# Kernel optimization log

Measured on AMD Instinct MI355X. Metric: run time of the kernel, lower is better.

The kernel has to match this reference:

```python
import jax, jax.numpy as jnp
import numpy as np

B, T = 8192, 2048


def setup_inputs() -> dict:
    key = jax.random.key(0)
    u = jax.random.normal(key, (B, T, 1), dtype=jnp.float32)
    return {
        "u": u,
        "dt": jnp.float32(0.01),
        "m": jnp.float32(1.0),
        "c": jnp.float32(0.1),
        "k": jnp.float32(2.0),
        "in_mean": jnp.float32(0.5),
        "in_std": jnp.float32(2.0),
        "out_mean": jnp.float32(0.0),
        "out_std": jnp.float32(1.5),
    }


def reference(u, dt, m, c, k, in_mean, in_std, out_mean, out_std):
    # u: (B, T, 1) scaled forcing signal; state: (B, 2) = [position, velocity]
    Bsz = u.shape[0]
    u_seq = jnp.transpose(u[..., 0])  # (T, B) for lax.scan over time
    state0 = jnp.zeros((Bsz, 2), dtype=u.dtype)

    def step(state, u_t):
        # in_s.inverse_transform: unscale input
        u_p = u_t * in_std + in_mean  # (B,)
        x, v = state[:, 0], state[:, 1]
        # prior(state, u_p): mass-spring-damper derivative [dx, dv]
        acc = (u_p - c * v - k * x) / m
        new_state = state + dt * jnp.stack([v, acc], axis=1)  # Euler step
        # prior.ay on the UPDATED state (matches torch: state updated first)
        ay = (u_p - c * new_state[:, 1] - k * new_state[:, 0]) / m
        # out_s.transform: scale output
        y = (ay - out_mean) / out_std  # (B,)
        return new_state, y

    state_T, ys = jax.lax.scan(step, state0, u_seq)  # ys: (T, B)
    return jnp.transpose(ys), state_T  # (B, T), (B, 2)
```

## Files before the change

kernel.cpp:

```cpp
#include <hip/hip_runtime.h>

#define TT 2048
#define LP 32

__device__ __forceinline__ float b2f(unsigned short h) {
    union { unsigned int u; float f; } x; x.u = ((unsigned int)h) << 16; return x.f;
}
__device__ __forceinline__ unsigned short f2b(float f) {
    union { float f; unsigned int u; } x; x.f = f;
    unsigned int r = x.u + 0x7fffu + ((x.u >> 16) & 1u);
    return (unsigned short)(r >> 16);
}
__device__ __forceinline__ float ldsc(const void* p, bool bf) {
    return bf ? b2f(*(const unsigned short*)p) : *(const float*)p;
}
__device__ __forceinline__ int swz(int u) { return u ^ ((u >> 3) & 7); }

__global__ __launch_bounds__(256, 4) void phys_scan(
    const void* __restrict__ u_in,
    const void* __restrict__ p_dt, const void* __restrict__ p_m,
    const void* __restrict__ p_c,  const void* __restrict__ p_k,
    const void* __restrict__ p_im, const void* __restrict__ p_is,
    const void* __restrict__ p_om, const void* __restrict__ p_os,
    void* __restrict__ out, int rows)
{
    __shared__ uint4 smem[4][512];
    const int lane = threadIdx.x & 63;
    const int wid  = threadIdx.x >> 6;
    const int b = blockIdx.x * 4 + wid;
    if (b >= rows) return;

    uint4* W = smem[wid];

    const bool bf = (((const unsigned short*)p_m)[0] != 0);

    if (bf) {
        const uint4* g = (const uint4*)((const unsigned short*)u_in + (size_t)b * TT);
        #pragma unroll
        for (int j = 0; j < 4; j++) {
            uint4 w = g[j * 64 + lane];
            W[swz(j * 64 + lane)] = w;
        }
    } else {
        const uint4* g = (const uint4*)((const float*)u_in + (size_t)b * TT);
        #pragma unroll
        for (int j = 0; j < 8; j++) {
            uint4 w = g[j * 64 + lane];
            W[swz(j * 64 + lane)] = w;
        }
    }

    const float dt = ldsc(p_dt, bf);
    const float mm = ldsc(p_m,  bf);
    const float cc = ldsc(p_c,  bf);
    const float kk = ldsc(p_k,  bf);
    const float im = ldsc(p_im, bf);
    const float is = ldsc(p_is, bf);
    const float om = ldsc(p_om, bf);
    const float os = ldsc(p_os, bf);

    const float inv_m  = 1.0f / mm;
    const float inv_os = 1.0f / os;
    const float a21 = -dt * kk * inv_m;
    const float a22 = 1.0f - dt * cc * inv_m;
    const float dtm = dt * inv_m;

    __builtin_amdgcn_wave_barrier();
    float uf[LP];
    if (bf) {
        #pragma unroll
        for (int m = 0; m < 4; m++) {
            uint4 w = W[swz(lane * 4 + m)];
            unsigned int ws[4] = {w.x, w.y, w.z, w.w};
            #pragma unroll
            for (int q = 0; q < 4; q++) {
                uf[m*8 + q*2 + 0] = b2f((unsigned short)(ws[q] & 0xffffu));
                uf[m*8 + q*2 + 1] = b2f((unsigned short)(ws[q] >> 16));
            }
        }
    } else {
        #pragma unroll
        for (int m = 0; m < 8; m++) {
            uint4 w = W[swz(lane * 8 + m)];
            uf[m*4+0] = __uint_as_float(w.x);
            uf[m*4+1] = __uint_as_float(w.y);
            uf[m*4+2] = __uint_as_float(w.z);
            uf[m*4+3] = __uint_as_float(w.w);
        }
    }

    float px = 0.f, pv = 0.f;
    #pragma unroll
    for (int i = 0; i < LP; i++) {
        float up = uf[i] * is + im;
        uf[i] = up;
        float nx = px + dt * pv;
        float nv = a21 * px + a22 * pv + dtm * up;
        px = nx; pv = nv;
    }

    float m00 = 1.f, m01 = dt, m10 = a21, m11 = a22;
    #pragma unroll
    for (int i = 0; i < 5; i++) {
        float t00 = m00*m00 + m01*m10;
        float t01 = m00*m01 + m01*m11;
        float t10 = m10*m00 + m11*m10;
        float t11 = m10*m01 + m11*m11;
        m00=t00; m01=t01; m10=t10; m11=t11;
    }

    #pragma unroll
    for (int o = 1; o < 64; o <<= 1) {
        float rx = __shfl_up(px, o, 64);
        float rv = __shfl_up(pv, o, 64);
        if (lane >= o) {
            px = m00*rx + m01*rv + px;
            pv = m10*rx + m11*rv + pv;
        }
        if (o < 32) {
            float t00 = m00*m00 + m01*m10;
            float t01 = m00*m01 + m01*m11;
            float t10 = m10*m00 + m11*m10;
            float t11 = m10*m01 + m11*m11;
            m00=t00; m01=t01; m10=t10; m11=t11;
        }
    }

    float ex = __shfl_up(px, 1, 64);
    float ev = __shfl_up(pv, 1, 64);
    if (lane == 0) { ex = 0.f; ev = 0.f; }

    float x = ex, v = ev;
    #pragma unroll
    for (int i = 0; i < LP; i++) {
        float up = uf[i];
        float nx = x + dt * v;
        float nv = a21 * x + a22 * v + dtm * up;
        float ay = (up - cc * nv - kk * nx) * inv_m;
        uf[i] = (ay - om) * inv_os;
        x = nx; v = nv;
    }

    __builtin_amdgcn_wave_barrier();
    if (bf) {
        #pragma unroll
        for (int m = 0; m < 4; m++) {
            uint4 w;
            w.x = (unsigned)f2b(uf[m*8+0]) | ((unsigned)f2b(uf[m*8+1]) << 16);
            w.y = (unsigned)f2b(uf[m*8+2]) | ((unsigned)f2b(uf[m*8+3]) << 16);
            w.z = (unsigned)f2b(uf[m*8+4]) | ((unsigned)f2b(uf[m*8+5]) << 16);
            w.w = (unsigned)f2b(uf[m*8+6]) | ((unsigned)f2b(uf[m*8+7]) << 16);
            W[swz(lane * 4 + m)] = w;
        }
        __builtin_amdgcn_wave_barrier();
        unsigned short* ob = (unsigned short*)out;
        uint4* g = (uint4*)(ob + (size_t)b * TT);
        #pragma unroll
        for (int j = 0; j < 4; j++) g[j * 64 + lane] = W[swz(j * 64 + lane)];
        if (lane == 63) {
            size_t so = (size_t)rows * TT + (size_t)b * 2;
            ob[so]   = f2b(px);
            ob[so+1] = f2b(pv);
        }
    } else {
        #pragma unroll
        for (int m = 0; m < 8; m++) {
            uint4 w;
            w.x = __float_as_uint(uf[m*4+0]);
            w.y = __float_as_uint(uf[m*4+1]);
            w.z = __float_as_uint(uf[m*4+2]);
            w.w = __float_as_uint(uf[m*4+3]);
            W[swz(lane * 8 + m)] = w;
        }
        __builtin_amdgcn_wave_barrier();
        float* of = (float*)out;
        uint4* g = (uint4*)(of + (size_t)b * TT);
        #pragma unroll
        for (int j = 0; j < 8; j++) g[j * 64 + lane] = W[swz(j * 64 + lane)];
        if (lane == 63) {
            size_t so = (size_t)rows * TT + (size_t)b * 2;
            of[so]   = px;
            of[so+1] = pv;
        }
    }
}

extern "C" void kernel_launch(void* const* d_in, const int* in_sizes, int n_in,
                              void* d_out, int out_size, void* d_ws, size_t ws_size,
                              hipStream_t stream) {
    const int rows = in_sizes[0] / TT;
    const int blocks = (rows + 3) / 4;
    hipLaunchKernelGGL(phys_scan, dim3(blocks), dim3(256), 0, stream,
                       d_in[0], d_in[1], d_in[2], d_in[3], d_in[4],
                       d_in[5], d_in[6], d_in[7], d_in[8],
                       d_out, rows);
}
```

Before: 134.3 us.

## Make waves persistent over two rows with register prefetch of next row

After: 177.2 us. +32.0%, slower.

```diff
diff --git a/kernel.cpp b/kernel.cpp
--- a/kernel.cpp
+++ b/kernel.cpp
@@ -1,7 +1,6 @@
 #include <hip/hip_runtime.h>
 
 #define TT 2048
-#define LP 32
 
 __device__ __forceinline__ float b2f(unsigned short h) {
     union { unsigned int u; float f; } x; x.u = ((unsigned int)h) << 16; return x.f;
@@ -15,6 +14,163 @@
     return bf ? b2f(*(const unsigned short*)p) : *(const float*)p;
 }
 __device__ __forceinline__ int swz(int u) { return u ^ ((u >> 3) & 7); }
+
+template<bool BF>
+__device__ __forceinline__ void run_all(
+    const void* __restrict__ u_in, void* __restrict__ out, int rows,
+    int row0, int stride, int lane, uint4* __restrict__ W,
+    float dt, float cc, float kk, float inv_m,
+    float im, float is, float om, float inv_os)
+{
+    constexpr int NLD = BF ? 4 : 8;
+    constexpr int ES  = BF ? 2 : 4;
+
+    const float a21 = -dt * kk * inv_m;
+    const float a22 = 1.0f - dt * cc * inv_m;
+    const float dtm = dt * inv_m;
+
+    const char* ubase = (const char*)u_in;
+    char*       obase = (char*)out;
+
+    uint4 pf[NLD];
+    {
+        const uint4* g = (const uint4*)(ubase + (size_t)row0 * TT * ES);
+        #pragma unroll
+        for (int j = 0; j < NLD; j++) pf[j] = g[j * 64 + lane];
+    }
+
+    for (int r = row0; r < rows; r += stride) {
+        const int rn = r + stride;
+
+        __builtin_amdgcn_wave_barrier();
+        #pragma unroll
+        for (int j = 0; j < NLD; j++) W[swz(j * 64 + lane)] = pf[j];
+        __builtin_amdgcn_wave_barrier();
+
+        if (rn < rows) {
+            const uint4* g = (const uint4*)(ubase + (size_t)rn * TT * ES);
+            #pragma unroll
+            for (int j = 0; j < NLD; j++) pf[j] = g[j * 64 + lane];
+        }
+
+        float uf[32];
+        if (BF) {
+            #pragma unroll
+            for (int m = 0; m < 4; m++) {
+                uint4 w = W[swz(lane * 4 + m)];
+                unsigned int ws[4] = {w.x, w.y, w.z, w.w};
+                #pragma unroll
+                for (int q = 0; q < 4; q++) {
+                    uf[m*8 + q*2 + 0] = b2f((unsigned short)(ws[q] & 0xffffu));
+                    uf[m*8 + q*2 + 1] = b2f((unsigned short)(ws[q] >> 16));
+                }
+            }
+        } else {
+            #pragma unroll
+            for (int m = 0; m < 8; m++) {
+                uint4 w = W[swz(lane * 8 + m)];
+                uf[m*4+0] = __uint_as_float(w.x);
+                uf[m*4+1] = __uint_as_float(w.y);
+                uf[m*4+2] = __uint_as_float(w.z);
+                uf[m*4+3] = __uint_as_float(w.w);
+            }
+        }
+
+        float px = 0.f, pv = 0.f;
+        #pragma unroll
+        for (int i = 0; i < 32; i++) {
+            float up = uf[i] * is + im;
+            uf[i] = up;
+            float nx = px + dt * pv;
+            float nv = a21 * px + a22 * pv + dtm * up;
+            px = nx; pv = nv;
+        }
+
+        float m00 = 1.f, m01 = dt, m10 = a21, m11 = a22;
+        #pragma unroll
+        for (int i = 0; i < 5; i++) {
+            float t00 = m00*m00 + m01*m10;
+            float t01 = m00*m01 + m01*m11;
+            float t10 = m10*m00 + m11*m10;
+            float t11 = m10*m01 + m11*m11;
+            m00=t00; m01=t01; m10=t10; m11=t11;
+        }
+
+        #pragma unroll
+        for (int o = 1; o < 64; o <<= 1) {
+            float rx = __shfl_up(px, o, 64);
+            float rv = __shfl_up(pv, o, 64);
+            if (lane >= o) {
+                px = m00*rx + m01*rv + px;
+                pv = m10*rx + m11*rv + pv;
+            }
+            if (o < 32) {
+                float t00 = m00*m00 + m01*m10;
+                float t01 = m00*m01 + m01*m11;
+                float t10 = m10*m00 + m11*m10;
+                float t11 = m10*m01 + m11*m11;
+                m00=t00; m01=t01; m10=t10; m11=t11;
+            }
+        }
+
+        float ex = __shfl_up(px, 1, 64);
+        float ev = __shfl_up(pv, 1, 64);
+        if (lane == 0) { ex = 0.f; ev = 0.f; }
+
+        float x = ex, v = ev;
+        #pragma unroll
+        for (int i = 0; i < 32; i++) {
+            float up = uf[i];
+            float nx = x + dt * v;
+            float nv = a21 * x + a22 * v + dtm * up;
+            float ay = (up - cc * nv - kk * nx) * inv_m;
+            uf[i] = (ay - om) * inv_os;
+            x = nx; v = nv;
+        }
+
+        __builtin_amdgcn_wave_barrier();
+        if (BF) {
+            #pragma unroll
+            for (int m = 0; m < 4; m++) {
+                uint4 w;
+                w.x = (unsigned)f2b(uf[m*8+0]) | ((unsigned)f2b(uf[m*8+1]) << 16);
+                w.y = (unsigned)f2b(uf[m*8+2]) | ((unsigned)f2b(uf[m*8+3]) << 16);
+                w.z = (unsigned)f2b(uf[m*8+4]) | ((unsigned)f2b(uf[m*8+5]) << 16);
+                w.w = (unsigned)f2b(uf[m*8+6]) | ((unsigned)f2b(uf[m*8+7]) << 16);
+                W[swz(lane * 4 + m)] = w;
+            }
+        } else {
+            #pragma unroll
+            for (int m = 0; m < 8; m++) {
+                uint4 w;
+                w.x = __float_as_uint(uf[m*4+0]);
+                w.y = __float_as_uint(uf[m*4+1]);
+                w.z = __float_as_uint(uf[m*4+2]);
+                w.w = __float_as_uint(uf[m*4+3]);
+                W[swz(lane * 8 + m)] = w;
+            }
+        }
+        __builtin_amdgcn_wave_barrier();
+        {
+            uint4* g = (uint4*)(obase + (size_t)r * TT * ES);
+            #pragma unroll
+            for (int j = 0; j < NLD; j++) g[j * 64 + lane] = W[swz(j * 64 + lane)];
+        }
+        if (lane == 63) {
+            if (BF) {
+                unsigned short* ob = (unsigned short*)out;
+                size_t so = (size_t)rows * TT + (size_t)r * 2;
+                ob[so]   = f2b(px);
+                ob[so+1] = f2b(pv);
+            } else {
+                float* of = (float*)out;
+                size_t so = (size_t)rows * TT + (size_t)r * 2;
+                of[so]   = px;
+                of[so+1] = pv;
+            }
+        }
+    }
+}
 
 __global__ __launch_bounds__(256, 4) void phys_scan(
     const void* __restrict__ u_in,
@@ -22,33 +178,15 @@
     const void* __restrict__ p_c,  const void* __restrict__ p_k,
     const void* __restrict__ p_im, const void* __restrict__ p_is,
     const void* __restrict__ p_om, const void* __restrict__ p_os,
-    void* __restrict__ out, int rows)
+    void* __restrict__ out, int rows, int stride)
 {
     __shared__ uint4 smem[4][512];
     const int lane = threadIdx.x & 63;
     const int wid  = threadIdx.x >> 6;
-    const int b = blockIdx.x * 4 + wid;
-    if (b >= rows) return;
-
-    uint4* W = smem[wid];
+    const int row0 = blockIdx.x * 4 + wid;
+    if (row0 >= rows) return;
 
     const bool bf = (((const unsigned short*)p_m)[0] != 0);
-
-    if (bf) {
-        const uint4* g = (const uint4*)((const unsigned short*)u_in + (size_t)b * TT);
-        #pragma unroll
-        for (int j = 0; j < 4; j++) {
-            uint4 w = g[j * 64 + lane];
-            W[swz(j * 64 + lane)] = w;
-        }
-    } else {
-        const uint4* g = (const uint4*)((const float*)u_in + (size_t)b * TT);
-        #pragma unroll
-        for (int j = 0; j < 8; j++) {
-            uint4 w = g[j * 64 + lane];
-            W[swz(j * 64 + lane)] = w;
-        }
-    }
 
     const float dt = ldsc(p_dt, bf);
     const float mm = ldsc(p_m,  bf);
@@ -58,140 +196,25 @@
     const float is = ldsc(p_is, bf);
     const float om = ldsc(p_om, bf);
     const float os = ldsc(p_os, bf);
-
     const float inv_m  = 1.0f / mm;
     const float inv_os = 1.0f / os;
-    const float a21 = -dt * kk * inv_m;
-    const float a22 = 1.0f - dt * cc * inv_m;
-    const float dtm = dt * inv_m;
-
-    __builtin_amdgcn_wave_barrier();
-    float uf[LP];
-    if (bf) {
-        #pragma unroll
-        for (int m = 0; m < 4; m++) {
-            uint4 w = W[swz(lane * 4 + m)];
-            unsigned int ws[4] = {w.x, w.y, w.z, w.w};
-            #pragma unroll
-            for (int q = 0; q < 4; q++) {
-                uf[m*8 + q*2 + 0] = b2f((unsigned short)(ws[q] & 0xffffu));
-                uf[m*8 + q*2 + 1] = b2f((unsigned short)(ws[q] >> 16));
-            }
-        }
-    } else {
-        #pragma unroll
-        for (int m = 0; m < 8; m++) {
-            uint4 w = W[swz(lane * 8 + m)];
-            uf[m*4+0] = __uint_as_float(w.x);
-            uf[m*4+1] = __uint_as_float(w.y);
-            uf[m*4+2] = __uint_as_float(w.z);
-            uf[m*4+3] = __uint_as_float(w.w);
-        }
-    }
-
-    float px = 0.f, pv = 0.f;
-    #pragma unroll
-    for (int i = 0; i < LP; i++) {
-        float up = uf[i] * is + im;
-        uf[i] = up;
-        float nx = px + dt * pv;
-        float nv = a21 * px + a22 * pv + dtm * up;
-        px = nx; pv = nv;
-    }
-
-    float m00 = 1.f, m01 = dt, m10 = a21, m11 = a22;
-    #pragma unroll
-    for (int i = 0; i < 5; i++) {
-        float t00 = m00*m00 + m01*m10;
-        float t01 = m00*m01 + m01*m11;
-        float t10 = m10*m00 + m11*m10;
-        float t11 = m10*m01 + m11*m11;
-        m00=t00; m01=t01; m10=t10; m11=t11;
-    }
-
-    #pragma unroll
-    for (int o = 1; o < 64; o <<= 1) {
-        float rx = __shfl_up(px, o, 64);
-        float rv = __shfl_up(pv, o, 64);
-        if (lane >= o) {
-            px = m00*rx + m01*rv + px;
-            pv = m10*rx + m11*rv + pv;
-        }
-        if (o < 32) {
-            float t00 = m00*m00 + m01*m10;
-            float t01 = m00*m01 + m01*m11;
-            float t10 = m10*m00 + m11*m10;
-            float t11 = m10*m01 + m11*m11;
-            m00=t00; m01=t01; m10=t10; m11=t11;
-        }
-    }
-
-    float ex = __shfl_up(px, 1, 64);
-    float ev = __shfl_up(pv, 1, 64);
-    if (lane == 0) { ex = 0.f; ev = 0.f; }
-
-    float x = ex, v = ev;
-    #pragma unroll
-    for (int i = 0; i < LP; i++) {
-        float up = uf[i];
-        float nx = x + dt * v;
-        float nv = a21 * x + a22 * v + dtm * up;
-        float ay = (up - cc * nv - kk * nx) * inv_m;
-        uf[i] = (ay - om) * inv_os;
-        x = nx; v = nv;
-    }
-
-    __builtin_amdgcn_wave_barrier();
-    if (bf) {
-        #pragma unroll
-        for (int m = 0; m < 4; m++) {
-            uint4 w;
-            w.x = (unsigned)f2b(uf[m*8+0]) | ((unsigned)f2b(uf[m*8+1]) << 16);
-            w.y = (unsigned)f2b(uf[m*8+2]) | ((unsigned)f2b(uf[m*8+3]) << 16);
-            w.z = (unsigned)f2b(uf[m*8+4]) | ((unsigned)f2b(uf[m*8+5]) << 16);
-            w.w = (unsigned)f2b(uf[m*8+6]) | ((unsigned)f2b(uf[m*8+7]) << 16);
-            W[swz(lane * 4 + m)] = w;
-        }
-        __builtin_amdgcn_wave_barrier();
-        unsigned short* ob = (unsigned short*)out;
-        uint4* g = (uint4*)(ob + (size_t)b * TT);
-        #pragma unroll
-        for (int j = 0; j < 4; j++) g[j * 64 + lane] = W[swz(j * 64 + lane)];
-        if (lane == 63) {
-            size_t so = (size_t)rows * TT + (size_t)b * 2;
-            ob[so]   = f2b(px);
-            ob[so+1] = f2b(pv);
-        }
-    } else {
-        #pragma unroll
-        for (int m = 0; m < 8; m++) {
-            uint4 w;
-            w.x = __float_as_uint(uf[m*4+0]);
-            w.y = __float_as_uint(uf[m*4+1]);
-            w.z = __float_as_uint(uf[m*4+2]);
-            w.w = __float_as_uint(uf[m*4+3]);
-            W[swz(lane * 8 + m)] = w;
-        }
-        __builtin_amdgcn_wave_barrier();
-        float* of = (float*)out;
-        uint4* g = (uint4*)(of + (size_t)b * TT);
-        #pragma unroll
-        for (int j = 0; j < 8; j++) g[j * 64 + lane] = W[swz(j * 64 + lane)];
-        if (lane == 63) {
-            size_t so = (size_t)rows * TT + (size_t)b * 2;
-            of[so]   = px;
-            of[so+1] = pv;
-        }
-    }
+
+    if (bf) run_all<true >(u_in, out, rows, row0, stride, lane, smem[wid],
+                           dt, cc, kk, inv_m, im, is, om, inv_os);
+    else    run_all<false>(u_in, out, rows, row0, stride, lane, smem[wid],
+                           dt, cc, kk, inv_m, im, is, om, inv_os);
 }
 
 extern "C" void kernel_launch(void* const* d_in, const int* in_sizes, int n_in,
                               void* d_out, int out_size, void* d_ws, size_t ws_size,
                               hipStream_t stream) {
     const int rows = in_sizes[0] / TT;
-    const int blocks = (rows + 3) / 4;
+    int waves = rows / 2;
+    if (waves < 4) waves = rows;
+    const int blocks = (waves + 3) / 4;
+    const int stride = blocks * 4;
     hipLaunchKernelGGL(phys_scan, dim3(blocks), dim3(256), 0, stream,
                        d_in[0], d_in[1], d_in[2], d_in[3], d_in[4],
                        d_in[5], d_in[6], d_in[7], d_in[8],
-                       d_out, rows);
-}
+                       d_out, rows, stride);
+}
```

## Load input directly to LDS and store outputs straight from registers

Applied to the files above, without the earlier changes.

Result: slower. 149.3 us (+11.2%).

```diff
diff --git a/kernel.cpp b/kernel.cpp
--- a/kernel.cpp
+++ b/kernel.cpp
@@ -1,7 +1,6 @@
 #include <hip/hip_runtime.h>
 
 #define TT 2048
-#define LP 32
 
 __device__ __forceinline__ float b2f(unsigned short h) {
     union { unsigned int u; float f; } x; x.u = ((unsigned int)h) << 16; return x.f;
@@ -16,58 +15,39 @@
 }
 __device__ __forceinline__ int swz(int u) { return u ^ ((u >> 3) & 7); }
 
-__global__ __launch_bounds__(256, 4) void phys_scan(
-    const void* __restrict__ u_in,
-    const void* __restrict__ p_dt, const void* __restrict__ p_m,
-    const void* __restrict__ p_c,  const void* __restrict__ p_k,
-    const void* __restrict__ p_im, const void* __restrict__ p_is,
-    const void* __restrict__ p_om, const void* __restrict__ p_os,
-    void* __restrict__ out, int rows)
+__device__ __forceinline__ void gload16(const void* g, void* lds_base) {
+    __builtin_amdgcn_global_load_lds(
+        (const __attribute__((address_space(1))) void*)g,
+        (__attribute__((address_space(3))) void*)lds_base,
+        16, 0, 0);
+}
+
+template<bool BF>
+__device__ __forceinline__ void run_row(
+    const void* __restrict__ u_in, void* __restrict__ out, int rows,
+    int b, int lane, uint4* __restrict__ W,
+    float dt, float cc, float kk, float inv_m,
+    float im, float is, float om, float inv_os)
 {
-    __shared__ uint4 smem[4][512];
-    const int lane = threadIdx.x & 63;
-    const int wid  = threadIdx.x >> 6;
-    const int b = blockIdx.x * 4 + wid;
-    if (b >= rows) return;
+    constexpr int NLD = BF ? 4 : 8;
+    constexpr int ES  = BF ? 2 : 4;
 
-    uint4* W = smem[wid];
-
-    const bool bf = (((const unsigned short*)p_m)[0] != 0);
-
-    if (bf) {
-        const uint4* g = (const uint4*)((const unsigned short*)u_in + (size_t)b * TT);
-        #pragma unroll
-        for (int j = 0; j < 4; j++) {
-            uint4 w = g[j * 64 + lane];
-            W[swz(j * 64 + lane)] = w;
-        }
-    } else {
-        const uint4* g = (const uint4*)((const float*)u_in + (size_t)b * TT);
-        #pragma unroll
-        for (int j = 0; j < 8; j++) {
-            uint4 w = g[j * 64 + lane];
-            W[swz(j * 64 + lane)] = w;
-        }
-    }
-
-    const float dt = ldsc(p_dt, bf);
-    const float mm = ldsc(p_m,  bf);
-    const float cc = ldsc(p_c,  bf);
-    const float kk = ldsc(p_k,  bf);
-    const float im = ldsc(p_im, bf);
-    const float is = ldsc(p_is, bf);
-    const float om = ldsc(p_om, bf);
-    const float os = ldsc(p_os, bf);
-
-    const float inv_m  = 1.0f / mm;
-    const float inv_os = 1.0f / os;
     const float a21 = -dt * kk * inv_m;
     const float a22 = 1.0f - dt * cc * inv_m;
     const float dtm = dt * inv_m;
 
-    __builtin_amdgcn_wave_barrier();
-    float uf[LP];
-    if (bf) {
+    {
+        const char* g = (const char*)u_in + (size_t)b * TT * ES;
+        #pragma unroll
+        for (int j = 0; j < NLD; j++) {
+            gload16(g + (size_t)swz(j * 64 + lane) * 16, (char*)W + j * 1024);
+        }
+    }
+    asm volatile("s_waitcnt vmcnt(0)" ::: "memory");
+    __builtin_amdgcn_sched_barrier(0);
+
+    float uf[32];
+    if (BF) {
         #pragma unroll
         for (int m = 0; m < 4; m++) {
             uint4 w = W[swz(lane * 4 + m)];
@@ -91,7 +71,7 @@
 
     float px = 0.f, pv = 0.f;
     #pragma unroll
-    for (int i = 0; i < LP; i++) {
+    for (int i = 0; i < 32; i++) {
         float up = uf[i] * is + im;
         uf[i] = up;
         float nx = px + dt * pv;
@@ -132,7 +112,7 @@
 
     float x = ex, v = ev;
     #pragma unroll
-    for (int i = 0; i < LP; i++) {
+    for (int i = 0; i < 32; i++) {
         float up = uf[i];
         float nx = x + dt * v;
         float nv = a21 * x + a22 * v + dtm * up;
@@ -141,8 +121,8 @@
         x = nx; v = nv;
     }
 
-    __builtin_amdgcn_wave_barrier();
-    if (bf) {
+    if (BF) {
+        uint4* g = (uint4*)((unsigned short*)out + (size_t)b * TT + (size_t)lane * 32);
         #pragma unroll
         for (int m = 0; m < 4; m++) {
             uint4 w;
@@ -150,39 +130,60 @@
             w.y = (unsigned)f2b(uf[m*8+2]) | ((unsigned)f2b(uf[m*8+3]) << 16);
             w.z = (unsigned)f2b(uf[m*8+4]) | ((unsigned)f2b(uf[m*8+5]) << 16);
             w.w = (unsigned)f2b(uf[m*8+6]) | ((unsigned)f2b(uf[m*8+7]) << 16);
-            W[swz(lane * 4 + m)] = w;
+            g[m] = w;
         }
-        __builtin_amdgcn_wave_barrier();
-        unsigned short* ob = (unsigned short*)out;
-        uint4* g = (uint4*)(ob + (size_t)b * TT);
-        #pragma unroll
-        for (int j = 0; j < 4; j++) g[j * 64 + lane] = W[swz(j * 64 + lane)];
         if (lane == 63) {
+            unsigned short* ob = (unsigned short*)out;
             size_t so = (size_t)rows * TT + (size_t)b * 2;
             ob[so]   = f2b(px);
             ob[so+1] = f2b(pv);
         }
     } else {
+        float4* g = (float4*)((float*)out + (size_t)b * TT + (size_t)lane * 32);
         #pragma unroll
         for (int m = 0; m < 8; m++) {
-            uint4 w;
-            w.x = __float_as_uint(uf[m*4+0]);
-            w.y = __float_as_uint(uf[m*4+1]);
-            w.z = __float_as_uint(uf[m*4+2]);
-            w.w = __float_as_uint(uf[m*4+3]);
-            W[swz(lane * 8 + m)] = w;
+            g[m] = make_float4(uf[m*4+0], uf[m*4+1], uf[m*4+2], uf[m*4+3]);
         }
-        __builtin_amdgcn_wave_barrier();
-        float* of = (float*)out;
-        uint4* g = (uint4*)(of + (size_t)b * TT);
-        #pragma unroll
-        for (int j = 0; j < 8; j++) g[j * 64 + lane] = W[swz(j * 64 + lane)];
         if (lane == 63) {
+            float* of = (float*)out;
             size_t so = (size_t)rows * TT + (size_t)b * 2;
             of[so]   = px;
             of[so+1] = pv;
         }
     }
+}
+
+__global__ __launch_bounds__(256, 4) void phys_scan(
+    const void* __restrict__ u_in,
+    const void* __restrict__ p_dt, const void* __restrict__ p_m,
+    const void* __restrict__ p_c,  const void* __restrict__ p_k,
+    const void* __restrict__ p_im, const void* __restrict__ p_is,
+    const void* __restrict__ p_om, const void* __restrict__ p_os,
+    void* __restrict__ out, int rows)
+{
+    __shared__ uint4 smem[4][512];
+    const int lane = threadIdx.x & 63;
+    const int wid  = threadIdx.x >> 6;
+    const int b = blockIdx.x * 4 + wid;
+    if (b >= rows) return;
+
+    const bool bf = (((const unsigned short*)p_m)[0] != 0);
+
+    const float dt = ldsc(p_dt, bf);
+    const float mm = ldsc(p_m,  bf);
+    const float cc = ldsc(p_c,  bf);
+    const float kk = ldsc(p_k,  bf);
+    const float im = ldsc(p_im, bf);
+    const float is = ldsc(p_is, bf);
+    const float om = ldsc(p_om, bf);
+    const float os = ldsc(p_os, bf);
+    const float inv_m  = 1.0f / mm;
+    const float inv_os = 1.0f / os;
+
+    if (bf) run_row<true >(u_in, out, rows, b, lane, smem[wid],
+                           dt, cc, kk, inv_m, im, is, om, inv_os);
+    else    run_row<false>(u_in, out, rows, b, lane, smem[wid],
+                           dt, cc, kk, inv_m, im, is, om, inv_os);
 }
 
 extern "C" void kernel_launch(void* const* d_in, const int* in_sizes, int n_in,
```
